# Performance work log

Measured on AMD Instinct MI355X. Metric: run time of the kernel, lower is better.

## Reference

```python
import jax, jax.numpy as jnp
import numpy as np

N = 100000   # nodes
E = 1600000  # edges (node pairs)
D = 64       # msg_feature_len
H = 128      # hidden width of gate/message MLPs


def setup_inputs() -> dict:
    key = jax.random.key(0)
    ks = jax.random.split(key, 10)
    s = 0.05
    return {
        "node_weights": jax.random.uniform(ks[0], (N, 1), dtype=jnp.float32),
        "node_prev_features": jax.random.normal(ks[1], (N, D), dtype=jnp.float32),
        "self_idx": jax.random.randint(ks[2], (E,), 0, N),
        "neighbor_idx": jax.random.randint(ks[3], (E,), 0, N),
        "gw1": jax.random.normal(ks[4], (2 * D, H), dtype=jnp.float32) * s,
        "gb1": jnp.zeros((H,), jnp.float32),
        "gw2": jax.random.normal(ks[5], (H, 1), dtype=jnp.float32) * s,
        "gb2": jnp.zeros((1,), jnp.float32),
        "mw1": jax.random.normal(ks[6], (2 * D, H), dtype=jnp.float32) * s,
        "mb1": jnp.zeros((H,), jnp.float32),
        "mw2": jax.random.normal(ks[7], (H, D), dtype=jnp.float32) * s,
        "mb2": jnp.zeros((D,), jnp.float32),
        "pow_p": jax.random.normal(ks[8], (1,), dtype=jnp.float32),
    }


def reference(node_weights, node_prev_features, self_idx, neighbor_idx,
              gw1, gb1, gw2, gb2, mw1, mb1, mw2, mb2, pow_p):
    # gather + concat: message [E, 2D]
    msg = jnp.concatenate(
        [node_prev_features[self_idx], node_prev_features[neighbor_idx]], axis=1)
    w = node_weights[neighbor_idx]  # [E, 1]

    # gate MLP (Linear -> ReLU -> Linear): [E, 1]
    gate = jax.nn.relu(msg @ gw1 + gb1) @ gw2 + gb2
    # segment-softmax over edges grouped by self_idx, weighted by w**pow
    gmax = jax.ops.segment_max(gate, self_idx, num_segments=N)  # [N, 1]
    gate = (w ** pow_p) * jnp.exp(gate - gmax[self_idx])
    gsum = jax.ops.segment_sum(gate, self_idx, num_segments=N)  # [N, 1]
    gate = gate / (gsum[self_idx] + 1e-10)

    # message MLP: [E, D]
    x = jax.nn.relu(msg @ mw1 + mb1) @ mw2 + mb2

    # weighted scatter-sum back to nodes; single head -> mean is identity
    node_update = jax.ops.segment_sum(gate * x, self_idx, num_segments=N)
    return node_update + node_prev_features
```

## Files before the change

kernel.cpp:

```cpp
#include <hip/hip_runtime.h>
#include <hip/hip_bf16.h>

typedef __bf16 bf16x8 __attribute__((ext_vector_type(8)));
typedef float f32x4 __attribute__((ext_vector_type(4)));
typedef float f32x2 __attribute__((ext_vector_type(2)));

#define WIN 64
#define TILE 112
#define CHUNK 7
#define HSTR 136
#define SCAN_BLK 1024
#define SENT 0x7f7f7f7f

static __device__ __forceinline__ void dec8(unsigned x, unsigned y, float* o) {
    f32x2 a = __builtin_amdgcn_cvt_pk_f32_fp8(x, false);
    f32x2 b = __builtin_amdgcn_cvt_pk_f32_fp8(x, true);
    f32x2 c = __builtin_amdgcn_cvt_pk_f32_fp8(y, false);
    f32x2 d = __builtin_amdgcn_cvt_pk_f32_fp8(y, true);
    o[0] = a[0]; o[1] = a[1]; o[2] = b[0]; o[3] = b[1];
    o[4] = c[0]; o[5] = c[1]; o[6] = d[0]; o[7] = d[1];
}

__global__ void k_wconv(const float* __restrict__ gw1, const float* __restrict__ mw1,
                        const float* __restrict__ mw2,
                        __bf16* __restrict__ Bt, __bf16* __restrict__ mw2t,
                        int* __restrict__ hist, int* __restrict__ s_lo,
                        int* __restrict__ s_hi, int N, int NB)
{
    int i = blockIdx.x * 256 + threadIdx.x;
    if (i < 32768) {
        int c = i >> 6, k = i & 63;
        float v;
        if (c < 128)      v = gw1[k * 128 + c];
        else if (c < 256) v = gw1[(64 + k) * 128 + (c - 128)];
        else if (c < 384) v = mw1[k * 128 + (c - 256)];
        else              v = mw1[(64 + k) * 128 + (c - 384)];
        Bt[i] = (__bf16)v;
    } else if (i < 40960) {
        int j = i - 32768;
        int c = j >> 7, k = j & 127;
        mw2t[j] = (__bf16)mw2[k * 64 + c];
    }
    if (i < N) hist[i] = 0;
    if (i < NB) { s_lo[i] = SENT; s_hi[i] = 0; }
}

__global__ void __launch_bounds__(256, 4)
k_tab(const float* __restrict__ feat, const __bf16* __restrict__ Bt,
      const float* __restrict__ gb1, const float* __restrict__ mb1,
      const int* __restrict__ selfi, int* __restrict__ hist,
      unsigned char* __restrict__ Tp, unsigned char* __restrict__ Tq, int N, int E)
{
    __shared__ unsigned char ldsT[2][16][256];

    for (int e = blockIdx.x * 256 + threadIdx.x; e < E; e += gridDim.x * 256)
        atomicAdd(&hist[selfi[e]], 1);

    const int tid = threadIdx.x;
    const int lane = tid & 63, wv = tid >> 6;
    const int la = lane & 15, kg = lane >> 4;
    const int r0 = blockIdx.x * 16;
    if (r0 >= N) return;

    bf16x8 a[2];
    #pragma unroll
    for (int kk = 0; kk < 2; ++kk) {
        const int rr = min(r0 + la, N - 1);
        const float* src = feat + (size_t)rr * 64 + kk * 32 + kg * 8;
        f32x4 f0 = *reinterpret_cast<const f32x4*>(src);
        f32x4 f1 = *reinterpret_cast<const f32x4*>(src + 4);
        #pragma unroll
        for (int j = 0; j < 4; ++j) { a[kk][j] = (__bf16)f0[j]; a[kk][4 + j] = (__bf16)f1[j]; }
    }
    #pragma unroll
    for (int j = 0; j < 8; ++j) {
        const int c = wv * 128 + j * 16 + la;
        float bias = 0.f;
        if (c < 128) bias = gb1[c];
        else if (c >= 256 && c < 384) bias = mb1[c - 256];
        f32x4 acc = {bias, bias, bias, bias};
        #pragma unroll
        for (int kk = 0; kk < 2; ++kk) {
            bf16x8 bb = *reinterpret_cast<const bf16x8*>(Bt + (size_t)c * 64 + kk * 32 + kg * 8);
            acc = __builtin_amdgcn_mfma_f32_16x16x32_bf16(a[kk], bb, acc, 0, 0, 0);
        }
        int tbl, boff;
        if (c < 128)      { tbl = 0; boff = ((c) >> 3) * 16 + (c & 7); }
        else if (c < 256) { const int q = c - 128; tbl = 1; boff = (q >> 3) * 16 + (q & 7); }
        else if (c < 384) { const int q = c - 256; tbl = 0; boff = (q >> 3) * 16 + 8 + (q & 7); }
        else              { const int q = c - 384; tbl = 1; boff = (q >> 3) * 16 + 8 + (q & 7); }
        #pragma unroll
        for (int i = 0; i < 4; ++i) {
            const int pk = __builtin_amdgcn_cvt_pk_fp8_f32(acc[i], acc[i], 0, false);
            ldsT[tbl][kg * 4 + i][boff] = (unsigned char)(pk & 0xff);
        }
    }
    __syncthreads();
    {
        const int row = tid >> 4, v4 = tid & 15;
        if (r0 + row < N) {
            const uint4* s0p = reinterpret_cast<const uint4*>(&ldsT[0][row][0]);
            const uint4* s1p = reinterpret_cast<const uint4*>(&ldsT[1][row][0]);
            reinterpret_cast<uint4*>(Tp + (size_t)(r0 + row) * 256)[v4] = s0p[v4];
            reinterpret_cast<uint4*>(Tq + (size_t)(r0 + row) * 256)[v4] = s1p[v4];
        }
    }
}

__global__ void k_scan1(const int* __restrict__ hist, int* __restrict__ incl,
                        int* __restrict__ bsum, int N)
{
    __shared__ int sd[SCAN_BLK];
    int i = blockIdx.x * SCAN_BLK + threadIdx.x;
    int v = (i < N) ? hist[i] : 0;
    sd[threadIdx.x] = v;
    __syncthreads();
    for (int off = 1; off < SCAN_BLK; off <<= 1) {
        int t = (threadIdx.x >= off) ? sd[threadIdx.x - off] : 0;
        __syncthreads();
        sd[threadIdx.x] += t;
        __syncthreads();
    }
    if (i < N) incl[i] = sd[threadIdx.x];
    if (threadIdx.x == SCAN_BLK - 1) bsum[blockIdx.x] = sd[SCAN_BLK - 1];
}

__global__ void k_scan23(const int* __restrict__ incl, const int* __restrict__ hist,
                         const int* __restrict__ bsum,
                         int* __restrict__ cursor, int* __restrict__ starts,
                         int* __restrict__ s_lo, int* __restrict__ s_hi,
                         float* __restrict__ lpw, const float* __restrict__ nodew,
                         const float* __restrict__ powp,
                         const float* __restrict__ prev, float* __restrict__ out,
                         int N, int E)
{
    __shared__ int boff_s;
    if (threadIdx.x < 64) {
        int part = 0;
        for (int j = threadIdx.x; j < (int)blockIdx.x; j += 64) part += bsum[j];
        #pragma unroll
        for (int sh = 1; sh < 64; sh <<= 1) part += __shfl_xor(part, sh, 64);
        if (threadIdx.x == 0) boff_s = part;
    }
    __syncthreads();
    int i = blockIdx.x * SCAN_BLK + threadIdx.x;
    if (i >= N) return;
    const int h = hist[i];
    const int v = incl[i] - h + boff_s;
    cursor[i] = v;
    starts[i] = v;
    lpw[i] = powp[0] * __logf(nodew[i]);
    if (h > 0) {
        const int b = v / WIN;
        atomicMin(&s_lo[b], i);
        atomicMax(&s_hi[b], i + 1);
    } else {
        const float* ps = prev + (size_t)i * 64;
        float* po = out + (size_t)i * 64;
        for (int k = 0; k < 64; ++k) po[k] = ps[k];
    }
}

__global__ void k_scatter(const int* __restrict__ selfi, const int* __restrict__ nbri,
                          int* __restrict__ cursor, int* __restrict__ nbr_p, int E)
{
    int e = blockIdx.x * 256 + threadIdx.x;
    if (e >= E) return;
    int s = selfi[e];
    int pos = atomicAdd(&cursor[s], 1);
    nbr_p[pos] = nbri[e];
}

__global__ void __launch_bounds__(256, 5)
k_fused(const unsigned char* __restrict__ Tp, const unsigned char* __restrict__ Tq,
        const int* __restrict__ nbr_p, const int* __restrict__ starts,
        const int* __restrict__ s_lo, const int* __restrict__ s_hi,
        const float* __restrict__ lpw,
        const float* __restrict__ gw2, const float* __restrict__ gb2,
        const __bf16* __restrict__ mw2t, const float* __restrict__ mb2,
        const float* __restrict__ prev, float* __restrict__ out,
        int N, int E)
{
    __shared__ __align__(16) unsigned char hlds8[TILE][HSTR];
    __shared__ float logit_s[TILE];
    __shared__ float ginv_s[WIN];
    __shared__ int st_s[WIN + 1];

    const int b = blockIdx.x;
    const int s0 = s_lo[b];
    if (s0 == SENT) return;
    const int s1 = s_hi[b];
    const int nseg = s1 - s0;
    const int e0 = starts[s0];
    const int e1 = (s1 < N) ? starts[s1] : E;
    int ne = e1 - e0;
    if (ne > TILE) ne = TILE;

    const int tid = threadIdx.x;
    for (int j = tid; j <= nseg; j += 256)
        st_s[j] = (j < nseg) ? starts[s0 + j] : e1;
    __syncthreads();

    const int lane = tid & 63, wv = tid >> 6;
    const int g16 = tid >> 4, il = tid & 15;

    {
        const float b2v = gb2[0];
        float w2f[8];
        {
            f32x4 wa = *reinterpret_cast<const f32x4*>(gw2 + il * 8);
            f32x4 wb = *reinterpret_cast<const f32x4*>(gw2 + il * 8 + 4);
            w2f[0] = wa[0]; w2f[1] = wa[1]; w2f[2] = wa[2]; w2f[3] = wa[3];
            w2f[4] = wb[0]; w2f[5] = wb[1]; w2f[6] = wb[2]; w2f[7] = wb[3];
        }
        const int ck = (ne + 15) >> 4;
        const int rb = g16 * ck;
        const int re = min(rb + ck, ne);
        const int m = re - rb;
        if (m > 0) {
            uint4 qv[CHUNK];
            float lpv[CHUNK];
            #pragma unroll
            for (int j = 0; j < CHUNK; ++j) {
                const int rc = (j < m) ? (rb + j) : (re - 1);
                const int nn = nbr_p[e0 + rc];
                qv[j] = *reinterpret_cast<const uint4*>(Tq + (size_t)nn * 256 + il * 16);
                lpv[j] = lpw[nn];
            }
            int cur;
            {
                int lo = 0, hi = nseg - 1;
                while (lo < hi) {
                    const int mid = (lo + hi + 1) >> 1;
                    if (st_s[mid] <= e0 + rb) lo = mid; else hi = mid - 1;
                }
                cur = lo;
            }
            int curlim = st_s[cur + 1];
            float pgf[8], pmf[8];
            {
                const uint4 tpv = *reinterpret_cast<const uint4*>(Tp + (size_t)(s0 + cur) * 256 + il * 16);
                dec8(tpv.x, tpv.y, pgf);
                dec8(tpv.z, tpv.w, pmf);
            }
            #pragma unroll
            for (int j = 0; j < CHUNK; ++j) {
                if (j < m) {
                    const int r = rb + j;
                    if (e0 + r >= curlim) {
                        do { ++cur; curlim = st_s[cur + 1]; } while (e0 + r >= curlim);
                        const uint4 tpv = *reinterpret_cast<const uint4*>(Tp + (size_t)(s0 + cur) * 256 + il * 16);
                        dec8(tpv.x, tpv.y, pgf);
                        dec8(tpv.z, tpv.w, pmf);
                    }
                    float qgv[8], qmv[8];
                    dec8(qv[j].x, qv[j].y, qgv);
                    dec8(qv[j].z, qv[j].w, qmv);
                    float lg = 0.f;
                    float hm[8];
                    #pragma unroll
                    for (int q = 0; q < 8; ++q) {
                        lg = fmaf(fmaxf(pgf[q] + qgv[q], 0.f), w2f[q], lg);
                        hm[q] = fmaxf(pmf[q] + qmv[q], 0.f);
                    }
                    unsigned d0 = __builtin_amdgcn_cvt_pk_fp8_f32(hm[0], hm[1], 0, false);
                    d0 = __builtin_amdgcn_cvt_pk_fp8_f32(hm[2], hm[3], d0, true);
                    unsigned d1 = __builtin_amdgcn_cvt_pk_fp8_f32(hm[4], hm[5], 0, false);
                    d1 = __builtin_amdgcn_cvt_pk_fp8_f32(hm[6], hm[7], d1, true);
                    *reinterpret_cast<uint2*>(&hlds8[r][il * 8]) = make_uint2(d0, d1);
                    #pragma unroll
                    for (int sh = 1; sh < 16; sh <<= 1)
                        lg += __shfl_xor(lg, sh, 16);
                    if (il == 0) logit_s[r] = lg + b2v + lpv[j];
                }
            }
        }
    }
    __syncthreads();

    const int la = lane & 15, kg = lane >> 4;
    const int row0[2] = {wv * 16, 64 + wv * 16};
    const bool lv[2] = {row0[0] < ne, (wv < 3) && (row0[1] < ne)};

    f32x4 c2[2][4] = {};
    #pragma unroll
    for (int kk = 0; kk < 4; ++kk) {
        const int kboff = kk * 32 + kg * 8;
        bf16x8 a[2];
        #pragma unroll
        for (int m2 = 0; m2 < 2; ++m2)
            if (lv[m2]) {
                const uint2 hw = *reinterpret_cast<const uint2*>(&hlds8[row0[m2] + la][kboff]);
                float t[8];
                dec8(hw.x, hw.y, t);
                #pragma unroll
                for (int q = 0; q < 8; ++q) a[m2][q] = (__bf16)t[q];
            }
        #pragma unroll
        for (int n = 0; n < 4; ++n) {
            bf16x8 bb = *reinterpret_cast<const bf16x8*>(mw2t + (size_t)(n * 16 + la) * 128 + kboff);
            #pragma unroll
            for (int m2 = 0; m2 < 2; ++m2)
                if (lv[m2]) c2[m2][n] = __builtin_amdgcn_mfma_f32_16x16x32_bf16(a[m2], bb, c2[m2][n], 0, 0, 0);
        }
    }

    for (int j = g16; j < nseg; j += 16) {
        int a0 = st_s[j] - e0;
        int a1 = st_s[j + 1] - e0;
        if (a1 > ne) a1 = ne;
        float mx = -3.4e38f;
        for (int idx = a0 + il; idx < a1; idx += 16)
            mx = fmaxf(mx, logit_s[idx]);
        #pragma unroll
        for (int sh = 1; sh < 16; sh <<= 1)
            mx = fmaxf(mx, __shfl_xor(mx, sh, 16));
        float sum = 0.f;
        for (int idx = a0 + il; idx < a1; idx += 16) {
            const float g = __expf(logit_s[idx] - mx);
            logit_s[idx] = g;
            sum += g;
        }
        #pragma unroll
        for (int sh = 1; sh < 16; sh <<= 1)
            sum += __shfl_xor(sum, sh, 16);
        if (il == 0) ginv_s[j] = 1.f / (sum + 1e-10f);
    }
    __syncthreads();

    __bf16 (*xb)[68] = reinterpret_cast<__bf16(*)[68]>(&hlds8[0][0]);
    #pragma unroll
    for (int m2 = 0; m2 < 2; ++m2) {
        if (!lv[m2]) continue;
        #pragma unroll
        for (int n = 0; n < 4; ++n) {
            const float b2v = mb2[n * 16 + la];
            #pragma unroll
            for (int i = 0; i < 4; ++i) {
                const int row = row0[m2] + kg * 4 + i;
                const float v = (row < ne) ? logit_s[row] * (c2[m2][n][i] + b2v) : 0.f;
                xb[row][n * 16 + la] = (__bf16)v;
            }
        }
    }
    __syncthreads();

    for (int j = wv; j < nseg; j += 4) {
        int a0 = st_s[j] - e0;
        int a1 = st_s[j + 1] - e0;
        if (a1 > ne) a1 = ne;
        if (a1 <= a0) continue;
        float sum = 0.f;
        for (int r = a0; r < a1; ++r) sum += (float)xb[r][lane];
        const float gi = ginv_s[j];
        const size_t o = (size_t)(s0 + j) * 64 + lane;
        out[o] = prev[o] + sum * gi;
    }
}

extern "C" void kernel_launch(void* const* d_in, const int* in_sizes, int n_in,
                              void* d_out, int out_size, void* d_ws, size_t ws_size,
                              hipStream_t stream)
{
    const float* node_w = (const float*)d_in[0];
    const float* prev   = (const float*)d_in[1];
    const int*   selfi  = (const int*)d_in[2];
    const int*   nbri   = (const int*)d_in[3];
    const float* gw1 = (const float*)d_in[4];
    const float* gb1 = (const float*)d_in[5];
    const float* gw2 = (const float*)d_in[6];
    const float* gb2 = (const float*)d_in[7];
    const float* mw1 = (const float*)d_in[8];
    const float* mb1 = (const float*)d_in[9];
    const float* mw2 = (const float*)d_in[10];
    const float* mb2 = (const float*)d_in[11];
    const float* powp = (const float*)d_in[12];
    const int N = in_sizes[0];
    const int E = in_sizes[2];
    float* out = (float*)d_out;
    const int NB = (E + WIN - 1) / WIN;

    char* ws = (char*)d_ws;
    size_t off = 0;
    auto alloc = [&](size_t bytes) {
        void* p = ws + off;
        off = (off + bytes + 255) & ~(size_t)255;
        return p;
    };
    unsigned char* Tp    = (unsigned char*)alloc((size_t)N * 256);
    unsigned char* Tq    = (unsigned char*)alloc((size_t)N * 256);
    __bf16* Bt           = (__bf16*)alloc(512 * 64 * 2);
    __bf16* mw2t         = (__bf16*)alloc(64 * 128 * 2);
    int* nbr_p           = (int*)alloc((size_t)E * 4);
    int* hist            = (int*)alloc((size_t)N * 4);
    int* cursor          = (int*)alloc((size_t)N * 4);
    int* starts          = (int*)alloc((size_t)N * 4);
    int* incl            = (int*)alloc((size_t)N * 4);
    float* lpw           = (float*)alloc((size_t)N * 4);
    int* s_lo            = (int*)alloc((size_t)NB * 4);
    int* s_hi            = (int*)alloc((size_t)NB * 4);
    const int nb = (N + SCAN_BLK - 1) / SCAN_BLK;
    int* bsum            = (int*)alloc((size_t)nb * 4);

    int initN = N;
    if (initN < 40960) initN = 40960;
    if (initN < NB) initN = NB;
    k_wconv<<<(initN + 255) / 256, 256, 0, stream>>>(gw1, mw1, mw2, Bt, mw2t,
                                                     hist, s_lo, s_hi, N, NB);
    k_tab<<<(N + 15) / 16, 256, 0, stream>>>(prev, Bt, gb1, mb1, selfi, hist, Tp, Tq, N, E);
    k_scan1<<<nb, SCAN_BLK, 0, stream>>>(hist, incl, bsum, N);
    k_scan23<<<nb, SCAN_BLK, 0, stream>>>(incl, hist, bsum, cursor, starts, s_lo, s_hi,
                                          lpw, node_w, powp, prev, out, N, E);
    k_scatter<<<(E + 255) / 256, 256, 0, stream>>>(selfi, nbri, cursor, nbr_p, E);
    k_fused<<<NB, 256, 0, stream>>>(Tp, Tq, nbr_p, starts, s_lo, s_hi, lpw,
                                    gw2, gb2, mw2t, mb2, prev, out, N, E);
}
```

Measured before the change: 503.1 us.

## Stage neighbor rows into LDS via direct global-to-LDS loads, keep hidden in bf16

Neighbor projection rows (Tq) are now brought straight into a 256-byte-per-row LDS buffer with global_load_lds at kernel start, replacing per-thread register gathers. The same buffer is reused to hold the ReLU hidden activations as bf16, which drops the fp8 encode/decode round trip before the MFMA, and later holds the weighted message outputs as fp32. This is meant to cut register pressure and conversion work and to overlap the gathers with the st_s setup, at the cost of a larger LDS footprint (about 28KB versus about 15KB), which may reduce occupancy under launch_bounds(256,5).

New measurement: 544.4 us. +8.2%, slower.

```diff
diff --git a/kernel.cpp b/kernel.cpp
--- a/kernel.cpp
+++ b/kernel.cpp
@@ -8,7 +8,6 @@
 #define WIN 64
 #define TILE 112
 #define CHUNK 7
-#define HSTR 136
 #define SCAN_BLK 1024
 #define SENT 0x7f7f7f7f
 
@@ -19,6 +18,12 @@
     f32x2 d = __builtin_amdgcn_cvt_pk_f32_fp8(y, true);
     o[0] = a[0]; o[1] = a[1]; o[2] = b[0]; o[3] = b[1];
     o[4] = c[0]; o[5] = c[1]; o[6] = d[0]; o[7] = d[1];
+}
+
+static __device__ __forceinline__ void gl2lds16(const void* g, void* l) {
+    __builtin_amdgcn_global_load_lds(
+        (const __attribute__((address_space(1))) unsigned int*)g,
+        (__attribute__((address_space(3))) unsigned int*)l, 16, 0, 0);
 }
 
 __global__ void k_wconv(const float* __restrict__ gw1, const float* __restrict__ mw1,
@@ -181,7 +186,7 @@
         const float* __restrict__ prev, float* __restrict__ out,
         int N, int E)
 {
-    __shared__ __align__(16) unsigned char hlds8[TILE][HSTR];
+    __shared__ __align__(16) unsigned char ldsQ[TILE * 256];
     __shared__ float logit_s[TILE];
     __shared__ float ginv_s[WIN];
     __shared__ int st_s[WIN + 1];
@@ -197,12 +202,25 @@
     if (ne > TILE) ne = TILE;
 
     const int tid = threadIdx.x;
+    const int lane = tid & 63, wv = tid >> 6;
+    const int g16 = tid >> 4, il = tid & 15;
+    const int kg = lane >> 4;
+    const int ck = (ne + 15) >> 4;
+
+    {
+        const int rowbase = 4 * wv * ck;
+        for (int i = 0; i < ck; ++i) {
+            const int rbase = rowbase + 4 * i;
+            int r = rbase + (lane >> 4);
+            if (r > ne - 1) r = ne - 1;
+            const int nn = nbr_p[e0 + r];
+            gl2lds16(Tq + (size_t)nn * 256 + (size_t)(lane & 15) * 16,
+                     &ldsQ[rbase * 256]);
+        }
+    }
     for (int j = tid; j <= nseg; j += 256)
         st_s[j] = (j < nseg) ? starts[s0 + j] : e1;
     __syncthreads();
-
-    const int lane = tid & 63, wv = tid >> 6;
-    const int g16 = tid >> 4, il = tid & 15;
 
     {
         const float b2v = gb2[0];
@@ -213,19 +231,15 @@
             w2f[0] = wa[0]; w2f[1] = wa[1]; w2f[2] = wa[2]; w2f[3] = wa[3];
             w2f[4] = wb[0]; w2f[5] = wb[1]; w2f[6] = wb[2]; w2f[7] = wb[3];
         }
-        const int ck = (ne + 15) >> 4;
         const int rb = g16 * ck;
         const int re = min(rb + ck, ne);
         const int m = re - rb;
         if (m > 0) {
-            uint4 qv[CHUNK];
             float lpv[CHUNK];
             #pragma unroll
             for (int j = 0; j < CHUNK; ++j) {
                 const int rc = (j < m) ? (rb + j) : (re - 1);
-                const int nn = nbr_p[e0 + rc];
-                qv[j] = *reinterpret_cast<const uint4*>(Tq + (size_t)nn * 256 + il * 16);
-                lpv[j] = lpw[nn];
+                lpv[j] = lpw[nbr_p[e0 + rc]];
             }
             int cur;
             {
@@ -253,21 +267,18 @@
                         dec8(tpv.x, tpv.y, pgf);
                         dec8(tpv.z, tpv.w, pmf);
                     }
+                    const uint4 qq = *reinterpret_cast<const uint4*>(&ldsQ[r * 256 + il * 16]);
                     float qgv[8], qmv[8];
-                    dec8(qv[j].x, qv[j].y, qgv);
-                    dec8(qv[j].z, qv[j].w, qmv);
+                    dec8(qq.x, qq.y, qgv);
+                    dec8(qq.z, qq.w, qmv);
                     float lg = 0.f;
-                    float hm[8];
+                    bf16x8 hv;
                     #pragma unroll
                     for (int q = 0; q < 8; ++q) {
                         lg = fmaf(fmaxf(pgf[q] + qgv[q], 0.f), w2f[q], lg);
-                        hm[q] = fmaxf(pmf[q] + qmv[q], 0.f);
+                        hv[q] = (__bf16)fmaxf(pmf[q] + qmv[q], 0.f);
                     }
-                    unsigned d0 = __builtin_amdgcn_cvt_pk_fp8_f32(hm[0], hm[1], 0, false);
-                    d0 = __builtin_amdgcn_cvt_pk_fp8_f32(hm[2], hm[3], d0, true);
-                    unsigned d1 = __builtin_amdgcn_cvt_pk_fp8_f32(hm[4], hm[5], 0, false);
-                    d1 = __builtin_amdgcn_cvt_pk_fp8_f32(hm[6], hm[7], d1, true);
-                    *reinterpret_cast<uint2*>(&hlds8[r][il * 8]) = make_uint2(d0, d1);
+                    *reinterpret_cast<bf16x8*>(&ldsQ[r * 256 + il * 16]) = hv;
                     #pragma unroll
                     for (int sh = 1; sh < 16; sh <<= 1)
                         lg += __shfl_xor(lg, sh, 16);
@@ -278,27 +289,20 @@
     }
     __syncthreads();
 
-    const int la = lane & 15, kg = lane >> 4;
     const int row0[2] = {wv * 16, 64 + wv * 16};
     const bool lv[2] = {row0[0] < ne, (wv < 3) && (row0[1] < ne)};
 
     f32x4 c2[2][4] = {};
     #pragma unroll
     for (int kk = 0; kk < 4; ++kk) {
-        const int kboff = kk * 32 + kg * 8;
+        const int kboff = kk * 64 + kg * 16;
         bf16x8 a[2];
         #pragma unroll
         for (int m2 = 0; m2 < 2; ++m2)
-            if (lv[m2]) {
-                const uint2 hw = *reinterpret_cast<const uint2*>(&hlds8[row0[m2] + la][kboff]);
-                float t[8];
-                dec8(hw.x, hw.y, t);
-                #pragma unroll
-                for (int q = 0; q < 8; ++q) a[m2][q] = (__bf16)t[q];
-            }
+            if (lv[m2]) a[m2] = *reinterpret_cast<const bf16x8*>(&ldsQ[(row0[m2] + il) * 256 + kboff]);
         #pragma unroll
         for (int n = 0; n < 4; ++n) {
-            bf16x8 bb = *reinterpret_cast<const bf16x8*>(mw2t + (size_t)(n * 16 + la) * 128 + kboff);
+            bf16x8 bb = *reinterpret_cast<const bf16x8*>(mw2t + (size_t)(n * 16 + il) * 128 + kk * 32 + kg * 8);
             #pragma unroll
             for (int m2 = 0; m2 < 2; ++m2)
                 if (lv[m2]) c2[m2][n] = __builtin_amdgcn_mfma_f32_16x16x32_bf16(a[m2], bb, c2[m2][n], 0, 0, 0);
@@ -328,18 +332,17 @@
     }
     __syncthreads();
 
-    __bf16 (*xb)[68] = reinterpret_cast<__bf16(*)[68]>(&hlds8[0][0]);
     #pragma unroll
     for (int m2 = 0; m2 < 2; ++m2) {
         if (!lv[m2]) continue;
         #pragma unroll
         for (int n = 0; n < 4; ++n) {
-            const float b2v = mb2[n * 16 + la];
+            const float b2v = mb2[n * 16 + il];
             #pragma unroll
             for (int i = 0; i < 4; ++i) {
                 const int row = row0[m2] + kg * 4 + i;
                 const float v = (row < ne) ? logit_s[row] * (c2[m2][n][i] + b2v) : 0.f;
-                xb[row][n * 16 + la] = (__bf16)v;
+                *reinterpret_cast<float*>(&ldsQ[row * 256 + (n * 16 + il) * 4]) = v;
             }
         }
     }
@@ -351,7 +354,8 @@
         if (a1 > ne) a1 = ne;
         if (a1 <= a0) continue;
         float sum = 0.f;
-        for (int r = a0; r < a1; ++r) sum += (float)xb[r][lane];
+        for (int r = a0; r < a1; ++r)
+            sum += *reinterpret_cast<const float*>(&ldsQ[r * 256 + lane * 4]);
         const float gi = ginv_s[j];
         const size_t o = (size_t)(s0 + j) * 64 + lane;
         out[o] = prev[o] + sum * gi;
```
